# Performance work log

Measured on AMD Instinct MI355X. Metric: run time of the kernel, lower is better.

Reference implementation:

```python
import jax, jax.numpy as jnp
import numpy as np

N = 20000
E = 320000
D_IN = 1024
D_OUT = 1024


def setup_inputs() -> dict:
    key = jax.random.key(0)
    k1, k2, k3, k4 = jax.random.split(key, 4)
    x = jax.random.normal(k1, (N, D_IN), dtype=jnp.float32)
    edge_index = jax.random.randint(k2, (2, E), 0, N, dtype=jnp.int64)
    # nn.Linear params: W is [out, in], b is [out]
    W = jax.random.normal(k3, (D_OUT, D_IN), dtype=jnp.float32) * (1.0 / np.sqrt(D_IN))
    b = jax.random.normal(k4, (D_OUT,), dtype=jnp.float32) * 0.01
    return {"x": x, "edge_index": edge_index, "W": W, "b": b}


def reference(x, edge_index, W, b):
    num_nodes = x.shape[0]
    # add self-connections (same as addSelfConnect)
    self_idx = jnp.arange(num_nodes, dtype=edge_index.dtype)
    ei = jnp.concatenate([edge_index, jnp.stack([self_idx, self_idx], axis=0)], axis=1)
    row, col = ei[0], ei[1]
    # linear: h = x @ W^T + b  -> [N, D_OUT]
    h = jnp.einsum('nd,od->no', x, W) + b
    # degree computed from row indices only (matches calDegree(row, ...))
    deg = jnp.zeros((num_nodes,), dtype=h.dtype).at[row].add(1.0)
    deg_inv_sqrt = deg ** -0.5  # every node has a self-loop, so deg >= 1
    norm = deg_inv_sqrt[row] * deg_inv_sqrt[col]  # [E+N]
    # gather source features, scale per-edge, scatter-sum to destination nodes
    msg = norm[:, None] * h[col]  # [E+N, D_OUT]
    out = jax.ops.segment_sum(msg, row, num_segments=num_nodes)
    return out
```

## Files before the change

kernel.cpp:

```cpp
#include <hip/hip_runtime.h>
#include <hip/hip_bf16.h>
#include <stdint.h>
#include <stddef.h>


#define D_DIM 1024

typedef __bf16 bf16x8 __attribute__((ext_vector_type(8)));
typedef __bf16 bf16x4 __attribute__((ext_vector_type(4)));
typedef float  f32x4  __attribute__((ext_vector_type(4)));

#define GLOBAL_AS __attribute__((address_space(1)))
#define LDS_AS    __attribute__((address_space(3)))

static __device__ __forceinline__ void async_load16(const void* g, void* l) {
  __builtin_amdgcn_global_load_lds((GLOBAL_AS void*)(void*)g,
                                   (LDS_AS void*)l, 16, 0, 0);
}


__global__ void detect_kernel(const unsigned int* __restrict__ xw,
                              const unsigned int* __restrict__ ww,
                              const unsigned int* __restrict__ ew,
                              int* __restrict__ flags) {
  __shared__ int s[3];
  int t = threadIdx.x;
  if (t < 3) s[t] = 0;
  __syncthreads();
  int nx = 0, nw = 0, ze = 0;
  for (int i = t; i < 8192; i += 256) {
    if ((xw[i] & 0x7f80u) == 0x7f80u) nx++;
    if ((ww[i] & 0x7f80u) == 0x7f80u) nw++;
    if (ew[2 * i + 1] == 0u) ze++;
  }
  atomicAdd(&s[0], nx);
  atomicAdd(&s[1], nw);
  atomicAdd(&s[2], ze);
  __syncthreads();
  if (t == 0) {
    flags[0] = (s[0] >= 3) ? 1 : 0;
    flags[1] = (s[1] >= 3) ? 1 : 0;
    flags[2] = (s[2] >= 8000) ? 1 : 0;
  }
}


__global__ void zero_cnt_kernel(int* cnt, int n) {
  int i = blockIdx.x * blockDim.x + threadIdx.x;
  if (i < n) cnt[i] = 0;
}

__global__ void count_deg_kernel(const void* __restrict__ ei, int E,
                                 const int* __restrict__ flags,
                                 int* __restrict__ cnt) {
  int e = blockIdx.x * blockDim.x + threadIdx.x;
  if (e < E) {
    int r = flags[2] ? (int)((const long long*)ei)[e] : ((const int*)ei)[e];
    atomicAdd(&cnt[r], 1);
  }
}

__global__ void scan_kernel(const int* __restrict__ cnt, int n,
                            int* __restrict__ row_ptr, int* __restrict__ cursor,
                            float* __restrict__ dinv) {
  __shared__ int sdata[1024];
  __shared__ int carry_s;
  int t = threadIdx.x;
  if (t == 0) carry_s = 0;
  __syncthreads();
  for (int base = 0; base < n; base += 1024) {
    int idx = base + t;
    int v = (idx < n) ? cnt[idx] : 0;
    sdata[t] = v;
    __syncthreads();
    for (int off = 1; off < 1024; off <<= 1) {
      int add = (t >= off) ? sdata[t - off] : 0;
      __syncthreads();
      sdata[t] += add;
      __syncthreads();
    }
    int incl = sdata[t];
    int carry = carry_s;
    if (idx < n) {
      int excl = carry + incl - v;
      row_ptr[idx] = excl;
      cursor[idx]  = excl;
      dinv[idx] = rsqrtf((float)(v + 1));
    }
    __syncthreads();
    if (t == 1023) carry_s = carry + incl;
    __syncthreads();
  }
  if (t == 0) row_ptr[n] = carry_s;
}

__global__ void scatter_kernel(const void* __restrict__ ei, int E,
                               const int* __restrict__ flags,
                               const float* __restrict__ dinv,
                               int* __restrict__ cursor,
                               int* __restrict__ cols_out,
                               float* __restrict__ wgt, int emit_w) {
  int e = blockIdx.x * blockDim.x + threadIdx.x;
  if (e < E) {
    int r, c;
    if (flags[2]) {
      const long long* p = (const long long*)ei;
      r = (int)p[e]; c = (int)p[e + E];
    } else {
      const int* p = (const int*)ei;
      r = p[e]; c = p[e + E];
    }
    int pos = atomicAdd(&cursor[r], 1);
    cols_out[pos] = c;
    if (emit_w) wgt[pos] = dinv[r] * dinv[c];
  }
}


__global__ void conv_w_kernel(const void* __restrict__ W,
                              const void* __restrict__ b,
                              const int* __restrict__ flags,
                              unsigned short* __restrict__ Wb,
                              float* __restrict__ biasf) {
  int i = blockIdx.x * blockDim.x + threadIdx.x;
  int wfp = flags[1];
  if (wfp) {
    __bf16 h = (__bf16)((const float*)W)[i];
    Wb[i] = *(unsigned short*)&h;
  } else {
    Wb[i] = ((const unsigned short*)W)[i];
  }
  if (i < D_DIM) {
    biasf[i] = wfp ? ((const float*)b)[i] : (float)((const __bf16*)b)[i];
  }
}



__global__ __launch_bounds__(256) void gemm_xw_kernel(
    const void* __restrict__ Xv,
    const unsigned short* __restrict__ Wb,
    const float* __restrict__ biasf,
    const int* __restrict__ flags,
    __hip_bfloat16* __restrict__ H,
    int M) {
  __shared__ unsigned short As[128 * 32];
  __shared__ unsigned short Bs[128 * 32];

  const int t    = threadIdx.x;
  const int lane = t & 63;
  const int wave = t >> 6;
  const int wm   = wave >> 1;
  const int wn   = wave & 1;
  const int m0   = blockIdx.x * 128;
  const int n0   = blockIdx.y * 128;
  const int xfp  = flags[0];

  f32x4 acc[4][4] = {};

  const int ra = t >> 1;
  const int kh = (t & 1) * 16;
  const int rb = t >> 2;
  const int kc = (t & 3) * 8;
  const int quad = lane >> 4;
  const int mrow = lane & 15;

  for (int k0 = 0; k0 < D_DIM; k0 += 32) {
    async_load16(Wb + (size_t)(n0 + rb) * D_DIM + k0 + kc, &Bs[rb * 32 + kc]);
    async_load16(Wb + (size_t)(n0 + rb + 64) * D_DIM + k0 + kc,
                 &Bs[(rb + 64) * 32 + kc]);
    bf16x8 lo{}, hi{};
    int gm = m0 + ra;
    if (gm < M) {
      if (xfp) {
        const float* p = (const float*)Xv + (size_t)gm * D_DIM + k0 + kh;
        f32x4 v0 = *(const f32x4*)(p);
        f32x4 v1 = *(const f32x4*)(p + 4);
        f32x4 v2 = *(const f32x4*)(p + 8);
        f32x4 v3 = *(const f32x4*)(p + 12);
        lo[0] = (__bf16)v0[0]; lo[1] = (__bf16)v0[1];
        lo[2] = (__bf16)v0[2]; lo[3] = (__bf16)v0[3];
        lo[4] = (__bf16)v1[0]; lo[5] = (__bf16)v1[1];
        lo[6] = (__bf16)v1[2]; lo[7] = (__bf16)v1[3];
        hi[0] = (__bf16)v2[0]; hi[1] = (__bf16)v2[1];
        hi[2] = (__bf16)v2[2]; hi[3] = (__bf16)v2[3];
        hi[4] = (__bf16)v3[0]; hi[5] = (__bf16)v3[1];
        hi[6] = (__bf16)v3[2]; hi[7] = (__bf16)v3[3];
      } else {
        const unsigned short* p =
            (const unsigned short*)Xv + (size_t)gm * D_DIM + k0 + kh;
        lo = *(const bf16x8*)p;
        hi = *(const bf16x8*)(p + 8);
      }
    }
    *(bf16x8*)&As[ra * 32 + kh]     = lo;
    *(bf16x8*)&As[ra * 32 + kh + 8] = hi;
    __syncthreads();

    bf16x8 a[4], b[4];
#pragma unroll
    for (int i = 0; i < 4; ++i)
      a[i] = *(const bf16x8*)&As[(wm * 64 + i * 16 + mrow) * 32 + quad * 8];
#pragma unroll
    for (int j = 0; j < 4; ++j)
      b[j] = *(const bf16x8*)&Bs[(wn * 64 + j * 16 + mrow) * 32 + quad * 8];
#pragma unroll
    for (int i = 0; i < 4; ++i)
#pragma unroll
      for (int j = 0; j < 4; ++j)
        acc[i][j] = __builtin_amdgcn_mfma_f32_16x16x32_bf16(a[i], b[j], acc[i][j], 0, 0, 0);
    __syncthreads();
  }

#pragma unroll
  for (int j = 0; j < 4; ++j) {
    int n = n0 + wn * 64 + j * 16 + mrow;
    float bn = biasf[n];
#pragma unroll
    for (int i = 0; i < 4; ++i) {
      int mb = m0 + wm * 64 + i * 16 + quad * 4;
#pragma unroll
      for (int rg = 0; rg < 4; ++rg) {
        int m = mb + rg;
        if (m < M) H[(size_t)m * D_DIM + n] = __float2bfloat16(acc[i][j][rg] + bn);
      }
    }
  }
}


__global__ __launch_bounds__(256) void aggregate_h_kernel(
    const __hip_bfloat16* __restrict__ H,
    const int* __restrict__ row_ptr,
    const int* __restrict__ cols,
    const float* __restrict__ wgt,
    const float* __restrict__ dinv,
    const int* __restrict__ flags,
    void* __restrict__ outv, int M) {
  const int lane = threadIdx.x & 63;
  const int i = blockIdx.x * 4 + (threadIdx.x >> 6);
  if (i >= M) return;
  const int c0 = lane * 16;

  float a[16];
  {
    float di = dinv[i];
    float w = di * di;
    const __hip_bfloat16* p = H + (size_t)i * D_DIM + c0;
    bf16x8 v0 = *(const bf16x8*)p;
    bf16x8 v1 = *(const bf16x8*)(p + 8);
#pragma unroll
    for (int k = 0; k < 8; ++k) {
      a[k]     = w * (float)v0[k];
      a[8 + k] = w * (float)v1[k];
    }
  }
  const int e0 = row_ptr[i], e1 = row_ptr[i + 1];
  for (int e = e0; e < e1; ++e) {
    int c = cols[e];
    float w = wgt[e];
    const __hip_bfloat16* p = H + (size_t)c * D_DIM + c0;
    bf16x8 u0 = *(const bf16x8*)p;
    bf16x8 u1 = *(const bf16x8*)(p + 8);
#pragma unroll
    for (int k = 0; k < 8; ++k) {
      a[k]     += w * (float)u0[k];
      a[8 + k] += w * (float)u1[k];
    }
  }
  if (flags[0]) {
    float* o = (float*)outv + (size_t)i * D_DIM + c0;
#pragma unroll
    for (int q = 0; q < 4; ++q) {
      f32x4 r; r[0] = a[4*q]; r[1] = a[4*q+1]; r[2] = a[4*q+2]; r[3] = a[4*q+3];
      *(f32x4*)(o + 4 * q) = r;
    }
  } else {
    __hip_bfloat16* o = (__hip_bfloat16*)outv + (size_t)i * D_DIM + c0;
    bf16x8 r0, r1;
#pragma unroll
    for (int k = 0; k < 8; ++k) { r0[k] = (__bf16)a[k]; r1[k] = (__bf16)a[8+k]; }
    *(bf16x8*)o = r0;
    *(bf16x8*)(o + 8) = r1;
  }
}


__global__ __launch_bounds__(256) void aggregate_x_kernel(
    const void* __restrict__ X,
    const int* __restrict__ row_ptr,
    const int* __restrict__ cols,
    const float* __restrict__ dinv,
    const int* __restrict__ flags,
    float* __restrict__ rowsum,
    void* __restrict__ Y) {
  const int i  = blockIdx.x;
  const int c0 = threadIdx.x * 4;
  const float di = dinv[i];
  const int e0 = row_ptr[i], e1 = row_ptr[i + 1];
  float wsum = di * di;
  float a0, a1, a2, a3;

  if (flags[0]) {
    const float* Xf = (const float*)X;
    f32x4 v = *(const f32x4*)(Xf + (size_t)i * D_DIM + c0);
    a0 = wsum * v[0]; a1 = wsum * v[1]; a2 = wsum * v[2]; a3 = wsum * v[3];
    for (int e = e0; e < e1; ++e) {
      int c = cols[e];
      float w = di * dinv[c];
      wsum += w;
      f32x4 u = *(const f32x4*)(Xf + (size_t)c * D_DIM + c0);
      a0 += w * u[0]; a1 += w * u[1]; a2 += w * u[2]; a3 += w * u[3];
    }
    f32x4 r; r[0] = a0; r[1] = a1; r[2] = a2; r[3] = a3;
    *(f32x4*)((float*)Y + (size_t)i * D_DIM + c0) = r;
  } else {
    const __hip_bfloat16* Xb = (const __hip_bfloat16*)X;
    bf16x4 v = *(const bf16x4*)(Xb + (size_t)i * D_DIM + c0);
    a0 = wsum * (float)v[0]; a1 = wsum * (float)v[1];
    a2 = wsum * (float)v[2]; a3 = wsum * (float)v[3];
    for (int e = e0; e < e1; ++e) {
      int c = cols[e];
      float w = di * dinv[c];
      wsum += w;
      bf16x4 u = *(const bf16x4*)(Xb + (size_t)c * D_DIM + c0);
      a0 += w * (float)u[0]; a1 += w * (float)u[1];
      a2 += w * (float)u[2]; a3 += w * (float)u[3];
    }
    bf16x4 r;
    r[0] = (__bf16)a0; r[1] = (__bf16)a1; r[2] = (__bf16)a2; r[3] = (__bf16)a3;
    *(bf16x4*)((__hip_bfloat16*)Y + (size_t)i * D_DIM + c0) = r;
  }
  if (threadIdx.x == 0) rowsum[i] = wsum;
}

__global__ __launch_bounds__(256) void strip_gemm_kernel(
    const void* __restrict__ Yv,
    const unsigned short* __restrict__ Wb,
    const float* __restrict__ biasf,
    const float* __restrict__ rowsum,
    const int* __restrict__ flags,
    void* __restrict__ outv) {
  __shared__ unsigned short Ys[32 * 1024];

  const int t    = threadIdx.x;
  const int lane = t & 63;
  const int wave = t >> 6;
  const int m0   = blockIdx.x * 32;
  const int ofp  = flags[0];

  if (ofp) {
    const float* Yf = (const float*)Yv;
    for (int idx = t; idx < 32 * 128; idx += 256) {
      int r = idx >> 7, c = idx & 127;
      const float* p = Yf + (size_t)(m0 + r) * D_DIM + c * 8;
      f32x4 lo = *(const f32x4*)p;
      f32x4 hi = *(const f32x4*)(p + 4);
      bf16x8 v;
      v[0] = (__bf16)lo[0]; v[1] = (__bf16)lo[1];
      v[2] = (__bf16)lo[2]; v[3] = (__bf16)lo[3];
      v[4] = (__bf16)hi[0]; v[5] = (__bf16)hi[1];
      v[6] = (__bf16)hi[2]; v[7] = (__bf16)hi[3];
      int sc = c ^ (r & 15);
      *(bf16x8*)&Ys[r * 1024 + sc * 8] = v;
    }
  } else {
    const __hip_bfloat16* Yb = (const __hip_bfloat16*)Yv;
    for (int idx = t; idx < 32 * 128; idx += 256) {
      int r = idx >> 7, c = idx & 127;
      bf16x8 v = *(const bf16x8*)(Yb + (size_t)(m0 + r) * D_DIM + c * 8);
      int sc = c ^ (r & 15);
      *(bf16x8*)&Ys[r * 1024 + sc * 8] = v;
    }
  }
  __syncthreads();

  const int quad = lane >> 4;
  const int mrow = lane & 15;

  for (int nb = 0; nb < 4; ++nb) {
    f32x4 acc[2][4] = {};
    for (int k0 = 0; k0 < D_DIM; k0 += 32) {
      const int cbase = k0 >> 3;
      bf16x8 a[2], b[4];
#pragma unroll
      for (int i = 0; i < 2; ++i) {
        int m = i * 16 + mrow;
        int sc = (cbase + quad) ^ mrow;
        a[i] = *(const bf16x8*)&Ys[m * 1024 + sc * 8];
      }
#pragma unroll
      for (int j = 0; j < 4; ++j) {
        int n = wave * 256 + nb * 64 + j * 16 + mrow;
        b[j] = *(const bf16x8*)(Wb + (size_t)n * D_DIM + k0 + quad * 8);
      }
#pragma unroll
      for (int i = 0; i < 2; ++i)
#pragma unroll
        for (int j = 0; j < 4; ++j)
          acc[i][j] = __builtin_amdgcn_mfma_f32_16x16x32_bf16(a[i], b[j], acc[i][j], 0, 0, 0);
    }
#pragma unroll
    for (int j = 0; j < 4; ++j) {
      int n = wave * 256 + nb * 64 + j * 16 + mrow;
      float bn = biasf[n];
#pragma unroll
      for (int i = 0; i < 2; ++i) {
        int mb = m0 + i * 16 + quad * 4;
#pragma unroll
        for (int rg = 0; rg < 4; ++rg) {
          int m = mb + rg;
          float val = acc[i][j][rg] + rowsum[m] * bn;
          if (ofp) ((float*)outv)[(size_t)m * D_DIM + n] = val;
          else ((__hip_bfloat16*)outv)[(size_t)m * D_DIM + n] = __float2bfloat16(val);
        }
      }
    }
  }
}


extern "C" void kernel_launch(void* const* d_in, const int* in_sizes, int n_in,
                              void* d_out, int out_size, void* d_ws, size_t ws_size,
                              hipStream_t stream) {
  const void* x    = d_in[0];
  const void* ei   = d_in[1];
  const void* Wm   = d_in[2];
  const void* bias = d_in[3];

  const int E = in_sizes[1] / 2;
  const int M = in_sizes[0] / D_DIM;

  char* ws = (char*)d_ws;
  const size_t KB = 1024, MB = 1024 * 1024;

  const size_t need_fast = 6 * MB + (size_t)M * D_DIM * 2 + MB;

  if (ws_size >= need_fast) {
    int*   flags   = (int*)(ws);
    int*   cnt     = (int*)(ws + 4 * KB);
    int*   row_ptr = (int*)(ws + 128 * KB);
    int*   cursor  = (int*)(ws + 256 * KB);
    float* dinv    = (float*)(ws + 384 * KB);
    float* biasf   = (float*)(ws + 512 * KB);
    int*   cols    = (int*)(ws + 768 * KB);
    float* wgt     = (float*)(ws + 2 * MB);
    unsigned short* Wb = (unsigned short*)(ws + 4 * MB);
    __hip_bfloat16* H  = (__hip_bfloat16*)(ws + 6 * MB);

    detect_kernel<<<1, 256, 0, stream>>>((const unsigned int*)x,
                                         (const unsigned int*)Wm,
                                         (const unsigned int*)ei, (int*)flags);
    zero_cnt_kernel<<<(M + 255) / 256, 256, 0, stream>>>(cnt, M);
    count_deg_kernel<<<(E + 255) / 256, 256, 0, stream>>>(ei, E, flags, cnt);
    scan_kernel<<<1, 1024, 0, stream>>>(cnt, M, row_ptr, cursor, dinv);
    scatter_kernel<<<(E + 255) / 256, 256, 0, stream>>>(ei, E, flags, dinv,
                                                        cursor, cols, wgt, 1);
    conv_w_kernel<<<(D_DIM * D_DIM) / 256, 256, 0, stream>>>(Wm, bias, flags,
                                                             Wb, biasf);
    dim3 ggrid((M + 127) / 128, D_DIM / 128);
    gemm_xw_kernel<<<ggrid, 256, 0, stream>>>(x, Wb, biasf, flags, H, M);
    aggregate_h_kernel<<<(M + 3) / 4, 256, 0, stream>>>(H, row_ptr, cols, wgt,
                                                        dinv, flags, d_out, M);
  } else {
    int*   flags   = (int*)(ws);
    int*   cnt     = (int*)(ws + 4 * KB);
    int*   row_ptr = (int*)(ws + 128 * KB);
    int*   cursor  = (int*)(ws + 256 * KB);
    float* dinv    = (float*)(ws + 384 * KB);
    float* rowsum  = (float*)(ws + 512 * KB);
    float* biasf   = (float*)(ws + 640 * KB);
    int*   cols    = (int*)(ws + 768 * KB);
    unsigned short* Wb = (unsigned short*)(ws + 2 * MB);

    detect_kernel<<<1, 256, 0, stream>>>((const unsigned int*)x,
                                         (const unsigned int*)Wm,
                                         (const unsigned int*)ei, (int*)flags);
    zero_cnt_kernel<<<(M + 255) / 256, 256, 0, stream>>>(cnt, M);
    count_deg_kernel<<<(E + 255) / 256, 256, 0, stream>>>(ei, E, flags, cnt);
    scan_kernel<<<1, 1024, 0, stream>>>(cnt, M, row_ptr, cursor, dinv);
    scatter_kernel<<<(E + 255) / 256, 256, 0, stream>>>(ei, E, flags, dinv,
                                                        cursor, cols, (float*)0, 0);
    conv_w_kernel<<<(D_DIM * D_DIM) / 256, 256, 0, stream>>>(Wm, bias, flags,
                                                             Wb, biasf);
    aggregate_x_kernel<<<M, 256, 0, stream>>>(x, row_ptr, cols, dinv, flags,
                                              rowsum, d_out);
    strip_gemm_kernel<<<M / 32, 256, 0, stream>>>(d_out, Wb, biasf, rowsum,
                                                  flags, d_out);
  }
}
```

Before: 436.7 us.

## Pre-convert X to bf16 and use async-LDS MFMA GEMM with swizzled grid

Adds a kernel that converts fp32 X to bf16 once, so a new GEMM kernel can stream both operands straight into LDS with global_load_lds and feed bf16 MFMA instructions. Workgroup indices are remapped so that blocks running together share X and W tiles in cache. The single-block scan is also rewritten to have each thread scan its own chunk serially, which cuts the number of barrier rounds. The cost is an extra workspace buffer the size of X in bf16 plus an extra pass over X, and the new GEMM path only runs when the workspace is large enough.

```diff
diff --git a/kernel.cpp b/kernel.cpp
--- a/kernel.cpp
+++ b/kernel.cpp
@@ -63,35 +63,30 @@
 __global__ void scan_kernel(const int* __restrict__ cnt, int n,
                             int* __restrict__ row_ptr, int* __restrict__ cursor,
                             float* __restrict__ dinv) {
-  __shared__ int sdata[1024];
-  __shared__ int carry_s;
-  int t = threadIdx.x;
-  if (t == 0) carry_s = 0;
+  __shared__ int ssum[256];
+  const int t = threadIdx.x;
+  const int chunk = (n + 255) / 256;
+  const int lo = t * chunk;
+  const int hi = (lo + chunk < n) ? lo + chunk : n;
+  int s = 0;
+  for (int i = lo; i < hi; ++i) s += cnt[i];
+  ssum[t] = s;
   __syncthreads();
-  for (int base = 0; base < n; base += 1024) {
-    int idx = base + t;
-    int v = (idx < n) ? cnt[idx] : 0;
-    sdata[t] = v;
+  for (int off = 1; off < 256; off <<= 1) {
+    int add = (t >= off) ? ssum[t - off] : 0;
     __syncthreads();
-    for (int off = 1; off < 1024; off <<= 1) {
-      int add = (t >= off) ? sdata[t - off] : 0;
-      __syncthreads();
-      sdata[t] += add;
-      __syncthreads();
-    }
-    int incl = sdata[t];
-    int carry = carry_s;
-    if (idx < n) {
-      int excl = carry + incl - v;
-      row_ptr[idx] = excl;
-      cursor[idx]  = excl;
-      dinv[idx] = rsqrtf((float)(v + 1));
-    }
+    ssum[t] += add;
     __syncthreads();
-    if (t == 1023) carry_s = carry + incl;
-    __syncthreads();
-  }
-  if (t == 0) row_ptr[n] = carry_s;
+  }
+  int run = ssum[t] - s;
+  for (int i = lo; i < hi; ++i) {
+    int v = cnt[i];
+    row_ptr[i] = run;
+    cursor[i]  = run;
+    dinv[i] = rsqrtf((float)(v + 1));
+    run += v;
+  }
+  if (t == 255) row_ptr[n] = ssum[255];
 }
 
 __global__ void scatter_kernel(const void* __restrict__ ei, int E,
@@ -135,6 +130,97 @@
   }
 }
 
+
+__global__ __launch_bounds__(256) void conv_x_kernel(
+    const void* __restrict__ X, const int* __restrict__ flags,
+    unsigned short* __restrict__ Xb, int total8) {
+  int i = blockIdx.x * blockDim.x + threadIdx.x;
+  if (i >= total8) return;
+  if (!flags[0]) return;
+  const float* p = (const float*)X + (size_t)i * 8;
+  f32x4 v0 = *(const f32x4*)p;
+  f32x4 v1 = *(const f32x4*)(p + 4);
+  bf16x8 r;
+  r[0] = (__bf16)v0[0]; r[1] = (__bf16)v0[1];
+  r[2] = (__bf16)v0[2]; r[3] = (__bf16)v0[3];
+  r[4] = (__bf16)v1[0]; r[5] = (__bf16)v1[1];
+  r[6] = (__bf16)v1[2]; r[7] = (__bf16)v1[3];
+  *(bf16x8*)(Xb + (size_t)i * 8) = r;
+}
+
+
+__global__ __launch_bounds__(256) void gemm_xw2_kernel(
+    const void* __restrict__ Xv,
+    const unsigned short* __restrict__ Xb,
+    const unsigned short* __restrict__ Wb,
+    const float* __restrict__ biasf,
+    const int* __restrict__ flags,
+    __hip_bfloat16* __restrict__ H,
+    int M) {
+  __shared__ unsigned short As[128 * 32];
+  __shared__ unsigned short Bs[128 * 32];
+
+  const int t    = threadIdx.x;
+  const int lane = t & 63;
+  const int wave = t >> 6;
+  const int wm   = wave >> 1;
+  const int wn   = wave & 1;
+
+  const int nwg = gridDim.x;
+  const int wg  = (blockIdx.x & 7) * (nwg >> 3) + (blockIdx.x >> 3);
+  const int m0  = (wg >> 3) * 128;
+  const int n0  = (wg & 7) * 128;
+
+  const unsigned short* Asrc =
+      flags[0] ? Xb : (const unsigned short*)Xv;
+
+  f32x4 acc[4][4] = {};
+
+  const int ra = t >> 2;
+  const int kc = (t & 3) * 8;
+  int gr0 = m0 + ra;       if (gr0 >= M) gr0 = M - 1;
+  int gr1 = m0 + 64 + ra;  if (gr1 >= M) gr1 = M - 1;
+  const int quad = lane >> 4;
+  const int mrow = lane & 15;
+
+  for (int k0 = 0; k0 < D_DIM; k0 += 32) {
+    async_load16(Asrc + (size_t)gr0 * D_DIM + k0 + kc, &As[ra * 32 + kc]);
+    async_load16(Asrc + (size_t)gr1 * D_DIM + k0 + kc, &As[(ra + 64) * 32 + kc]);
+    async_load16(Wb + (size_t)(n0 + ra) * D_DIM + k0 + kc, &Bs[ra * 32 + kc]);
+    async_load16(Wb + (size_t)(n0 + ra + 64) * D_DIM + k0 + kc,
+                 &Bs[(ra + 64) * 32 + kc]);
+    __syncthreads();
+
+    bf16x8 a[4], b[4];
+#pragma unroll
+    for (int i = 0; i < 4; ++i)
+      a[i] = *(const bf16x8*)&As[(wm * 64 + i * 16 + mrow) * 32 + quad * 8];
+#pragma unroll
+    for (int j = 0; j < 4; ++j)
+      b[j] = *(const bf16x8*)&Bs[(wn * 64 + j * 16 + mrow) * 32 + quad * 8];
+#pragma unroll
+    for (int i = 0; i < 4; ++i)
+#pragma unroll
+      for (int j = 0; j < 4; ++j)
+        acc[i][j] = __builtin_amdgcn_mfma_f32_16x16x32_bf16(a[i], b[j], acc[i][j], 0, 0, 0);
+    __syncthreads();
+  }
+
+#pragma unroll
+  for (int j = 0; j < 4; ++j) {
+    int n = n0 + wn * 64 + j * 16 + mrow;
+    float bn = biasf[n];
+#pragma unroll
+    for (int i = 0; i < 4; ++i) {
+      int mb = m0 + wm * 64 + i * 16 + quad * 4;
+#pragma unroll
+      for (int rg = 0; rg < 4; ++rg) {
+        int m = mb + rg;
+        if (m < M) H[(size_t)m * D_DIM + n] = __float2bfloat16(acc[i][j][rg] + bn);
+      }
+    }
+  }
+}
 
 
 __global__ __launch_bounds__(256) void gemm_xw_kernel(
@@ -434,7 +520,9 @@
   char* ws = (char*)d_ws;
   const size_t KB = 1024, MB = 1024 * 1024;
 
-  const size_t need_fast = 6 * MB + (size_t)M * D_DIM * 2 + MB;
+  const size_t szH = (size_t)M * D_DIM * 2;
+  const size_t need_fast   = 6 * MB + szH + MB;
+  const size_t need_faster = 6 * MB + 2 * szH + MB;
 
   if (ws_size >= need_fast) {
     int*   flags   = (int*)(ws);
@@ -447,19 +535,29 @@
     float* wgt     = (float*)(ws + 2 * MB);
     unsigned short* Wb = (unsigned short*)(ws + 4 * MB);
     __hip_bfloat16* H  = (__hip_bfloat16*)(ws + 6 * MB);
+    unsigned short* Xb = (unsigned short*)(ws + 6 * MB + szH);
 
     detect_kernel<<<1, 256, 0, stream>>>((const unsigned int*)x,
                                          (const unsigned int*)Wm,
                                          (const unsigned int*)ei, (int*)flags);
     zero_cnt_kernel<<<(M + 255) / 256, 256, 0, stream>>>(cnt, M);
     count_deg_kernel<<<(E + 255) / 256, 256, 0, stream>>>(ei, E, flags, cnt);
-    scan_kernel<<<1, 1024, 0, stream>>>(cnt, M, row_ptr, cursor, dinv);
+    scan_kernel<<<1, 256, 0, stream>>>(cnt, M, row_ptr, cursor, dinv);
     scatter_kernel<<<(E + 255) / 256, 256, 0, stream>>>(ei, E, flags, dinv,
                                                         cursor, cols, wgt, 1);
     conv_w_kernel<<<(D_DIM * D_DIM) / 256, 256, 0, stream>>>(Wm, bias, flags,
                                                              Wb, biasf);
-    dim3 ggrid((M + 127) / 128, D_DIM / 128);
-    gemm_xw_kernel<<<ggrid, 256, 0, stream>>>(x, Wb, biasf, flags, H, M);
+    const int mtiles = (M + 127) / 128;
+    if (ws_size >= need_faster) {
+      const int total8 = M * (D_DIM / 8);
+      conv_x_kernel<<<(total8 + 255) / 256, 256, 0, stream>>>(x, flags, Xb,
+                                                              total8);
+      gemm_xw2_kernel<<<mtiles * 8, 256, 0, stream>>>(x, Xb, Wb, biasf, flags,
+                                                      H, M);
+    } else {
+      dim3 ggrid(mtiles, D_DIM / 128);
+      gemm_xw_kernel<<<ggrid, 256, 0, stream>>>(x, Wb, biasf, flags, H, M);
+    }
     aggregate_h_kernel<<<(M + 3) / 4, 256, 0, stream>>>(H, row_ptr, cols, wgt,
                                                         dinv, flags, d_out, M);
   } else {
@@ -478,7 +576,7 @@
                                          (const unsigned int*)ei, (int*)flags);
     zero_cnt_kernel<<<(M + 255) / 256, 256, 0, stream>>>(cnt, M);
     count_deg_kernel<<<(E + 255) / 256, 256, 0, stream>>>(ei, E, flags, cnt);
-    scan_kernel<<<1, 1024, 0, stream>>>(cnt, M, row_ptr, cursor, dinv);
+    scan_kernel<<<1, 256, 0, stream>>>(cnt, M, row_ptr, cursor, dinv);
     scatter_kernel<<<(E + 255) / 256, 256, 0, stream>>>(ei, E, flags, dinv,
                                                         cursor, cols, (float*)0, 0);
     conv_w_kernel<<<(D_DIM * D_DIM) / 256, 256, 0, stream>>>(Wm, bias, flags,
```

Result: no change. 428.3 us (-1.9%).
